# Kernel optimization log

Hardware: AMD Instinct MI355X
Metric: run time of the kernel (lower is better)

Reference implementation:

```python
import jax, jax.numpy as jnp
import numpy as np


def _demosaic_kernels():
    kgrb = 1/8 * np.array([[0,0,-1,0,0],[0,0,2,0,0],[-1,2,4,2,-1],[0,0,2,0,0],[0,0,-1,0,0]], dtype=np.float32)
    krbg0 = 1/8 * np.array([[0,0,0.5,0,0],[0,-1,0,-1,0],[-1,4,5,4,-1],[0,-1,0,-1,0],[0,0,0.5,0,0]], dtype=np.float32)
    krbg1 = krbg0.T
    krbbr = 1/8 * np.array([[0,0,-1.5,0,0],[0,2,0,2,0],[-1.5,0,6,0,-1.5],[0,2,0,2,0],[0,0,-1.5,0,0]], dtype=np.float32)
    return jnp.asarray(np.stack([kgrb, krbg0, krbg1, krbbr], 0)[:, None, :, :])  # (4,1,5,5)


def setup_inputs() -> dict:
    key = jax.random.key(0)
    x = jax.random.uniform(key, (4, 1, 2048, 2048), dtype=jnp.float32)  # RGGB bayer mosaic
    k = _demosaic_kernels()
    return {"x": x, "k": k}


def reference(x, k):
    # reflect-pad by 2 on H and W, then fixed 4-filter 5x5 conv
    xp = jnp.pad(x, ((0, 0), (0, 0), (2, 2), (2, 2)), mode="reflect")
    cfa = jax.lax.conv_general_dilated(
        xp, k, window_strides=(1, 1), padding="VALID",
        dimension_numbers=("NCHW", "OIHW", "NCHW"))  # (N,4,H,W)
    out = jnp.tile(x, (1, 3, 1, 1))  # (N,3,H,W)
    # green at R and B sites
    out = out.at[:, 1, 0::2, 0::2].set(cfa[:, 0, 0::2, 0::2])
    out = out.at[:, 1, 1::2, 1::2].set(cfa[:, 0, 1::2, 1::2])
    # red at G/B sites
    out = out.at[:, 0, 0::2, 1::2].set(cfa[:, 1, 0::2, 1::2])
    out = out.at[:, 0, 1::2, 0::2].set(cfa[:, 2, 1::2, 0::2])
    out = out.at[:, 0, 1::2, 1::2].set(cfa[:, 3, 1::2, 1::2])
    # blue at G/R sites
    out = out.at[:, 2, 0::2, 1::2].set(cfa[:, 2, 0::2, 1::2])
    out = out.at[:, 2, 1::2, 0::2].set(cfa[:, 1, 1::2, 0::2])
    out = out.at[:, 2, 0::2, 0::2].set(cfa[:, 3, 0::2, 0::2])
    return jnp.clip(out, 0.0, 1.0)
```

## Files before the change

### kernel.cpp

```cpp
#include <hip/hip_runtime.h>

#define IMG_H 2048
#define IMG_W 2048
#define NIMG 4

__device__ __forceinline__ int refl(int i, int n) {
    i = (i < 0) ? -i : i;
    return (i >= n) ? (2 * n - 2 - i) : i;
}

__device__ __forceinline__ float clamp01(float v) {
    return fminf(fmaxf(v, 0.0f), 1.0f);
}

__device__ __forceinline__ void px_rgb(
    float x0,
    float xl, float xr, float xll, float xrr,
    float xu, float xd, float xuu, float xdd,
    float dul, float dur, float ddl, float ddr,
    int pr, int pc,
    float& R, float& G, float& B)
{
    float h1 = xl + xr, v1 = xu + xd;
    float h2 = xll + xrr, v2 = xuu + xdd;
    float diag = dul + dur + ddl + ddr;
    float cfa0 = 0.125f * (4.0f * x0 + 2.0f * (h1 + v1) - (h2 + v2));
    float cfa1 = 0.125f * (5.0f * x0 + 4.0f * h1 - h2 + 0.5f * v2 - diag);
    float cfa2 = 0.125f * (5.0f * x0 + 4.0f * v1 - v2 + 0.5f * h2 - diag);
    float cfa3 = 0.125f * (6.0f * x0 + 2.0f * diag - 1.5f * (h2 + v2));

    if (pr == 0) {
        if (pc == 0) { R = x0;   G = cfa0; B = cfa3; }
        else         { R = cfa1; G = x0;   B = cfa2; }
    } else {
        if (pc == 0) { R = cfa2; G = x0;   B = cfa1; }
        else         { R = cfa3; G = cfa0; B = x0;   }
    }
    R = clamp01(R); G = clamp01(G); B = clamp01(B);
}

__global__ __launch_bounds__(256) void demosaic_interior(
    const float* __restrict__ x, float* __restrict__ out)
{
    int idx = blockIdx.x * blockDim.x + threadIdx.x;
    int c4   = idx & 511;
    int rest = idx >> 9;
    int rp   = rest & 1023;
    int n    = rest >> 10;
    if (rp == 0 || rp == 1023 || c4 == 0 || c4 == 511) return;
    int r = rp << 1;
    int c = c4 << 2;

    const float* p = x + (size_t)n * IMG_H * IMG_W;
    const size_t plane = (size_t)IMG_H * IMG_W;
    size_t ob = (size_t)n * 3 * plane + (size_t)r * IMG_W + c;

    const float* b = p + (size_t)r * IMG_W + c;
    float4 m2  = *(const float4*)(b - 2 * IMG_W);
    float4 m1l = *(const float4*)(b - IMG_W - 4);
    float4 m1c = *(const float4*)(b - IMG_W);
    float4 m1r = *(const float4*)(b - IMG_W + 4);
    float4 z0l = *(const float4*)(b - 4);
    float4 z0c = *(const float4*)(b);
    float4 z0r = *(const float4*)(b + 4);
    float4 z1l = *(const float4*)(b + IMG_W - 4);
    float4 z1c = *(const float4*)(b + IMG_W);
    float4 z1r = *(const float4*)(b + IMG_W + 4);
    float4 z2l = *(const float4*)(b + 2 * IMG_W - 4);
    float4 z2c = *(const float4*)(b + 2 * IMG_W);
    float4 z2r = *(const float4*)(b + 2 * IMG_W + 4);
    float4 p3  = *(const float4*)(b + 3 * IMG_W);

    float wm2[4] = {m2.x, m2.y, m2.z, m2.w};
    float wm1[6] = {m1l.w, m1c.x, m1c.y, m1c.z, m1c.w, m1r.x};
    float w0[8]  = {z0l.z, z0l.w, z0c.x, z0c.y, z0c.z, z0c.w, z0r.x, z0r.y};
    float w1[8]  = {z1l.z, z1l.w, z1c.x, z1c.y, z1c.z, z1c.w, z1r.x, z1r.y};
    float w2[6]  = {z2l.w, z2c.x, z2c.y, z2c.z, z2c.w, z2r.x};
    float w3[4]  = {p3.x, p3.y, p3.z, p3.w};

    float R0[4], G0[4], B0[4], R1[4], G1[4], B1[4];
    #pragma unroll
    for (int j = 0; j < 4; j++) {
        px_rgb(w0[j + 2],
               w0[j + 1], w0[j + 3], w0[j], w0[j + 4],
               wm1[j + 1], w1[j + 2], wm2[j], w2[j + 1],
               wm1[j], wm1[j + 2], w1[j + 1], w1[j + 3],
               0, j & 1, R0[j], G0[j], B0[j]);
        px_rgb(w1[j + 2],
               w1[j + 1], w1[j + 3], w1[j], w1[j + 4],
               w0[j + 2], w2[j + 1], wm1[j + 1], w3[j],
               w0[j + 1], w0[j + 3], w2[j], w2[j + 2],
               1, j & 1, R1[j], G1[j], B1[j]);
    }

    *(float4*)(out + ob)                     = make_float4(R0[0], R0[1], R0[2], R0[3]);
    *(float4*)(out + ob + plane)             = make_float4(G0[0], G0[1], G0[2], G0[3]);
    *(float4*)(out + ob + 2 * plane)         = make_float4(B0[0], B0[1], B0[2], B0[3]);
    *(float4*)(out + ob + IMG_W)             = make_float4(R1[0], R1[1], R1[2], R1[3]);
    *(float4*)(out + ob + IMG_W + plane)     = make_float4(G1[0], G1[1], G1[2], G1[3]);
    *(float4*)(out + ob + IMG_W + 2 * plane) = make_float4(B1[0], B1[1], B1[2], B1[3]);
}

__global__ __launch_bounds__(256) void demosaic_border(
    const float* __restrict__ x, float* __restrict__ out)
{
    const int PER_IMG = 1024 + 2044;
    int idx = blockIdx.x * blockDim.x + threadIdx.x;
    if (idx >= NIMG * PER_IMG) return;
    int n = idx / PER_IMG;
    int t = idx - n * PER_IMG;
    int rp, c4;
    if (t < 1024) { rp = (t >> 9) * 1023; c4 = t & 511; }
    else          { int j = t - 1024; rp = 1 + (j >> 1); c4 = (j & 1) * 511; }
    int r = rp << 1;
    int c = c4 << 2;

    const float* p = x + (size_t)n * IMG_H * IMG_W;
    const size_t plane = (size_t)IMG_H * IMG_W;
    size_t ob = (size_t)n * 3 * plane + (size_t)r * IMG_W + c;

    #pragma unroll
    for (int i = 0; i < 2; i++) {
        int rr = r + i;
        int rm1 = refl(rr - 1, IMG_H), rm2 = refl(rr - 2, IMG_H);
        int rp1 = refl(rr + 1, IMG_H), rp2 = refl(rr + 2, IMG_H);
        const float* p0r  = p + (size_t)rr  * IMG_W;
        const float* pm1r = p + (size_t)rm1 * IMG_W;
        const float* pm2r = p + (size_t)rm2 * IMG_W;
        const float* pp1r = p + (size_t)rp1 * IMG_W;
        const float* pp2r = p + (size_t)rp2 * IMG_W;
        #pragma unroll
        for (int j = 0; j < 4; j++) {
            int cc  = c + j;
            int cm1 = refl(cc - 1, IMG_W), cm2 = refl(cc - 2, IMG_W);
            int cp1 = refl(cc + 1, IMG_W), cp2 = refl(cc + 2, IMG_W);
            float R, G, B;
            px_rgb(p0r[cc],
                   p0r[cm1], p0r[cp1], p0r[cm2], p0r[cp2],
                   pm1r[cc], pp1r[cc], pm2r[cc], pp2r[cc],
                   pm1r[cm1], pm1r[cp1], pp1r[cm1], pp1r[cp1],
                   i, cc & 1, R, G, B);
            size_t o = ob + (size_t)i * IMG_W + j;
            out[o]             = R;
            out[o + plane]     = G;
            out[o + 2 * plane] = B;
        }
    }
}

extern "C" void kernel_launch(void* const* d_in, const int* in_sizes, int n_in,
                              void* d_out, int out_size, void* d_ws, size_t ws_size,
                              hipStream_t stream) {
    const float* x = (const float*)d_in[0];
    float* out = (float*)d_out;

    const int total = NIMG * (IMG_H / 2) * (IMG_W / 4);
    demosaic_interior<<<dim3(total / 256), dim3(256), 0, stream>>>(x, out);

    const int btotal = NIMG * (1024 + 2044);
    demosaic_border<<<dim3((btotal + 255) / 256), dim3(256), 0, stream>>>(x, out);
}
```

Before: 262.0 us.

## Merge interior and border kernels into one launch with XCD-aware block remapping

Combines the interior and border demosaic kernels into a single launch that dispatches on block index, removing one kernel launch and the gap between the two. Interior blocks are remapped so consecutive block IDs, which go round-robin to the 8 XCDs, cover contiguous image regions per XCD, so neighbouring rows share each XCD's L2. The border path's loops are no longer unrolled, keeping register pressure low in the shared kernel. Output stores are reordered by plane. The border work is tiny, so most of any effect should come from launch overhead and cache locality.

```diff
diff --git a/kernel.cpp b/kernel.cpp
--- a/kernel.cpp
+++ b/kernel.cpp
@@ -3,6 +3,12 @@
 #define IMG_H 2048
 #define IMG_W 2048
 #define NIMG 4
+#define NXCD 8
+
+#define NBLK_INT (NIMG * (IMG_H / 2) * (IMG_W / 4) / 256)
+#define PER_IMG  (1024 + 2044)
+#define NBORDER  (NIMG * PER_IMG)
+#define NBLK_BOR ((NBORDER + 255) / 256)
 
 __device__ __forceinline__ int refl(int i, int n) {
     i = (i < 0) ? -i : i;
@@ -39,111 +45,118 @@
     R = clamp01(R); G = clamp01(G); B = clamp01(B);
 }
 
-__global__ __launch_bounds__(256) void demosaic_interior(
+__global__ __launch_bounds__(256) void demosaic(
     const float* __restrict__ x, float* __restrict__ out)
 {
-    int idx = blockIdx.x * blockDim.x + threadIdx.x;
-    int c4   = idx & 511;
-    int rest = idx >> 9;
-    int rp   = rest & 1023;
-    int n    = rest >> 10;
-    if (rp == 0 || rp == 1023 || c4 == 0 || c4 == 511) return;
-    int r = rp << 1;
-    int c = c4 << 2;
+    const size_t plane = (size_t)IMG_H * IMG_W;
+    int bid = blockIdx.x;
 
-    const float* p = x + (size_t)n * IMG_H * IMG_W;
-    const size_t plane = (size_t)IMG_H * IMG_W;
-    size_t ob = (size_t)n * 3 * plane + (size_t)r * IMG_W + c;
+    if (bid < NBLK_INT) {
+        int nb  = (bid & (NXCD - 1)) * (NBLK_INT / NXCD) + (bid >> 3);
+        int idx = nb * 256 + (int)threadIdx.x;
 
-    const float* b = p + (size_t)r * IMG_W + c;
-    float4 m2  = *(const float4*)(b - 2 * IMG_W);
-    float4 m1l = *(const float4*)(b - IMG_W - 4);
-    float4 m1c = *(const float4*)(b - IMG_W);
-    float4 m1r = *(const float4*)(b - IMG_W + 4);
-    float4 z0l = *(const float4*)(b - 4);
-    float4 z0c = *(const float4*)(b);
-    float4 z0r = *(const float4*)(b + 4);
-    float4 z1l = *(const float4*)(b + IMG_W - 4);
-    float4 z1c = *(const float4*)(b + IMG_W);
-    float4 z1r = *(const float4*)(b + IMG_W + 4);
-    float4 z2l = *(const float4*)(b + 2 * IMG_W - 4);
-    float4 z2c = *(const float4*)(b + 2 * IMG_W);
-    float4 z2r = *(const float4*)(b + 2 * IMG_W + 4);
-    float4 p3  = *(const float4*)(b + 3 * IMG_W);
+        int c4   = idx & 511;
+        int rest = idx >> 9;
+        int rp   = rest & 1023;
+        int n    = rest >> 10;
+        if (rp == 0 || rp == 1023 || c4 == 0 || c4 == 511) return;
+        int r = rp << 1;
+        int c = c4 << 2;
 
-    float wm2[4] = {m2.x, m2.y, m2.z, m2.w};
-    float wm1[6] = {m1l.w, m1c.x, m1c.y, m1c.z, m1c.w, m1r.x};
-    float w0[8]  = {z0l.z, z0l.w, z0c.x, z0c.y, z0c.z, z0c.w, z0r.x, z0r.y};
-    float w1[8]  = {z1l.z, z1l.w, z1c.x, z1c.y, z1c.z, z1c.w, z1r.x, z1r.y};
-    float w2[6]  = {z2l.w, z2c.x, z2c.y, z2c.z, z2c.w, z2r.x};
-    float w3[4]  = {p3.x, p3.y, p3.z, p3.w};
+        const float* p = x + (size_t)n * IMG_H * IMG_W;
+        size_t ob = (size_t)n * 3 * plane + (size_t)r * IMG_W + c;
 
-    float R0[4], G0[4], B0[4], R1[4], G1[4], B1[4];
-    #pragma unroll
-    for (int j = 0; j < 4; j++) {
-        px_rgb(w0[j + 2],
-               w0[j + 1], w0[j + 3], w0[j], w0[j + 4],
-               wm1[j + 1], w1[j + 2], wm2[j], w2[j + 1],
-               wm1[j], wm1[j + 2], w1[j + 1], w1[j + 3],
-               0, j & 1, R0[j], G0[j], B0[j]);
-        px_rgb(w1[j + 2],
-               w1[j + 1], w1[j + 3], w1[j], w1[j + 4],
-               w0[j + 2], w2[j + 1], wm1[j + 1], w3[j],
-               w0[j + 1], w0[j + 3], w2[j], w2[j + 2],
-               1, j & 1, R1[j], G1[j], B1[j]);
-    }
+        const float* b = p + (size_t)r * IMG_W + c;
+        float4 m2  = *(const float4*)(b - 2 * IMG_W);
+        float4 m1l = *(const float4*)(b - IMG_W - 4);
+        float4 m1c = *(const float4*)(b - IMG_W);
+        float4 m1r = *(const float4*)(b - IMG_W + 4);
+        float4 z0l = *(const float4*)(b - 4);
+        float4 z0c = *(const float4*)(b);
+        float4 z0r = *(const float4*)(b + 4);
+        float4 z1l = *(const float4*)(b + IMG_W - 4);
+        float4 z1c = *(const float4*)(b + IMG_W);
+        float4 z1r = *(const float4*)(b + IMG_W + 4);
+        float4 z2l = *(const float4*)(b + 2 * IMG_W - 4);
+        float4 z2c = *(const float4*)(b + 2 * IMG_W);
+        float4 z2r = *(const float4*)(b + 2 * IMG_W + 4);
+        float4 p3  = *(const float4*)(b + 3 * IMG_W);
 
-    *(float4*)(out + ob)                     = make_float4(R0[0], R0[1], R0[2], R0[3]);
-    *(float4*)(out + ob + plane)             = make_float4(G0[0], G0[1], G0[2], G0[3]);
-    *(float4*)(out + ob + 2 * plane)         = make_float4(B0[0], B0[1], B0[2], B0[3]);
-    *(float4*)(out + ob + IMG_W)             = make_float4(R1[0], R1[1], R1[2], R1[3]);
-    *(float4*)(out + ob + IMG_W + plane)     = make_float4(G1[0], G1[1], G1[2], G1[3]);
-    *(float4*)(out + ob + IMG_W + 2 * plane) = make_float4(B1[0], B1[1], B1[2], B1[3]);
-}
+        float wm2[4] = {m2.x, m2.y, m2.z, m2.w};
+        float wm1[6] = {m1l.w, m1c.x, m1c.y, m1c.z, m1c.w, m1r.x};
+        float w0[8]  = {z0l.z, z0l.w, z0c.x, z0c.y, z0c.z, z0c.w, z0r.x, z0r.y};
+        float w1[8]  = {z1l.z, z1l.w, z1c.x, z1c.y, z1c.z, z1c.w, z1r.x, z1r.y};
+        float w2[6]  = {z2l.w, z2c.x, z2c.y, z2c.z, z2c.w, z2r.x};
+        float w3[4]  = {p3.x, p3.y, p3.z, p3.w};
 
-__global__ __launch_bounds__(256) void demosaic_border(
-    const float* __restrict__ x, float* __restrict__ out)
-{
-    const int PER_IMG = 1024 + 2044;
-    int idx = blockIdx.x * blockDim.x + threadIdx.x;
-    if (idx >= NIMG * PER_IMG) return;
-    int n = idx / PER_IMG;
-    int t = idx - n * PER_IMG;
-    int rp, c4;
-    if (t < 1024) { rp = (t >> 9) * 1023; c4 = t & 511; }
-    else          { int j = t - 1024; rp = 1 + (j >> 1); c4 = (j & 1) * 511; }
-    int r = rp << 1;
-    int c = c4 << 2;
-
-    const float* p = x + (size_t)n * IMG_H * IMG_W;
-    const size_t plane = (size_t)IMG_H * IMG_W;
-    size_t ob = (size_t)n * 3 * plane + (size_t)r * IMG_W + c;
-
-    #pragma unroll
-    for (int i = 0; i < 2; i++) {
-        int rr = r + i;
-        int rm1 = refl(rr - 1, IMG_H), rm2 = refl(rr - 2, IMG_H);
-        int rp1 = refl(rr + 1, IMG_H), rp2 = refl(rr + 2, IMG_H);
-        const float* p0r  = p + (size_t)rr  * IMG_W;
-        const float* pm1r = p + (size_t)rm1 * IMG_W;
-        const float* pm2r = p + (size_t)rm2 * IMG_W;
-        const float* pp1r = p + (size_t)rp1 * IMG_W;
-        const float* pp2r = p + (size_t)rp2 * IMG_W;
+        float R0[4], G0[4], B0[4], R1[4], G1[4], B1[4];
         #pragma unroll
         for (int j = 0; j < 4; j++) {
-            int cc  = c + j;
-            int cm1 = refl(cc - 1, IMG_W), cm2 = refl(cc - 2, IMG_W);
-            int cp1 = refl(cc + 1, IMG_W), cp2 = refl(cc + 2, IMG_W);
-            float R, G, B;
-            px_rgb(p0r[cc],
-                   p0r[cm1], p0r[cp1], p0r[cm2], p0r[cp2],
-                   pm1r[cc], pp1r[cc], pm2r[cc], pp2r[cc],
-                   pm1r[cm1], pm1r[cp1], pp1r[cm1], pp1r[cp1],
-                   i, cc & 1, R, G, B);
-            size_t o = ob + (size_t)i * IMG_W + j;
-            out[o]             = R;
-            out[o + plane]     = G;
-            out[o + 2 * plane] = B;
+            px_rgb(w0[j + 2],
+                   w0[j + 1], w0[j + 3], w0[j], w0[j + 4],
+                   wm1[j + 1], w1[j + 2], wm2[j], w2[j + 1],
+                   wm1[j], wm1[j + 2], w1[j + 1], w1[j + 3],
+                   0, j & 1, R0[j], G0[j], B0[j]);
+            px_rgb(w1[j + 2],
+                   w1[j + 1], w1[j + 3], w1[j], w1[j + 4],
+                   w0[j + 2], w2[j + 1], wm1[j + 1], w3[j],
+                   w0[j + 1], w0[j + 3], w2[j], w2[j + 2],
+                   1, j & 1, R1[j], G1[j], B1[j]);
+        }
+
+        *(float4*)(out + ob)                     = make_float4(R0[0], R0[1], R0[2], R0[3]);
+        *(float4*)(out + ob + IMG_W)             = make_float4(R1[0], R1[1], R1[2], R1[3]);
+        *(float4*)(out + ob + plane)             = make_float4(G0[0], G0[1], G0[2], G0[3]);
+        *(float4*)(out + ob + plane + IMG_W)     = make_float4(G1[0], G1[1], G1[2], G1[3]);
+        *(float4*)(out + ob + 2 * plane)         = make_float4(B0[0], B0[1], B0[2], B0[3]);
+        *(float4*)(out + ob + 2 * plane + IMG_W) = make_float4(B1[0], B1[1], B1[2], B1[3]);
+    } else {
+        int idx = (bid - NBLK_INT) * 256 + (int)threadIdx.x;
+        if (idx >= NBORDER) return;
+        int n = idx / PER_IMG;
+        int t = idx - n * PER_IMG;
+        int rp, c4;
+        if (t < 1024) { rp = (t >> 9) * 1023; c4 = t & 511; }
+        else          { int j = t - 1024; rp = 1 + (j >> 1); c4 = (j & 1) * 511; }
+        int r = rp << 1;
+        int c = c4 << 2;
+
+        const float* p = x + (size_t)n * IMG_H * IMG_W;
+        size_t ob = (size_t)n * 3 * plane + (size_t)r * IMG_W + c;
+
+        #pragma unroll 1
+        for (int i = 0; i < 2; i++) {
+            int rr = r + i;
+            int rm1 = refl(rr - 1, IMG_H), rm2 = refl(rr - 2, IMG_H);
+            int rp1 = refl(rr + 1, IMG_H), rp2 = refl(rr + 2, IMG_H);
+            const float* p0r  = p + (size_t)rr  * IMG_W;
+            const float* pm1r = p + (size_t)rm1 * IMG_W;
+            const float* pm2r = p + (size_t)rm2 * IMG_W;
+            const float* pp1r = p + (size_t)rp1 * IMG_W;
+            const float* pp2r = p + (size_t)rp2 * IMG_W;
+            #pragma unroll 1
+            for (int j = 0; j < 4; j++) {
+                int cc  = c + j;
+                int cm1 = refl(cc - 1, IMG_W), cm2 = refl(cc - 2, IMG_W);
+                int cp1 = refl(cc + 1, IMG_W), cp2 = refl(cc + 2, IMG_W);
+                float R, G, B;
+                if (i == 0)
+                    px_rgb(p0r[cc],
+                           p0r[cm1], p0r[cp1], p0r[cm2], p0r[cp2],
+                           pm1r[cc], pp1r[cc], pm2r[cc], pp2r[cc],
+                           pm1r[cm1], pm1r[cp1], pp1r[cm1], pp1r[cp1],
+                           0, cc & 1, R, G, B);
+                else
+                    px_rgb(p0r[cc],
+                           p0r[cm1], p0r[cp1], p0r[cm2], p0r[cp2],
+                           pm1r[cc], pp1r[cc], pm2r[cc], pp2r[cc],
+                           pm1r[cm1], pm1r[cp1], pp1r[cm1], pp1r[cp1],
+                           1, cc & 1, R, G, B);
+                size_t o = ob + (size_t)i * IMG_W + j;
+                out[o]             = R;
+                out[o + plane]     = G;
+                out[o + 2 * plane] = B;
+            }
         }
     }
 }
@@ -154,9 +167,5 @@
     const float* x = (const float*)d_in[0];
     float* out = (float*)d_out;
 
-    const int total = NIMG * (IMG_H / 2) * (IMG_W / 4);
-    demosaic_interior<<<dim3(total / 256), dim3(256), 0, stream>>>(x, out);
-
-    const int btotal = NIMG * (1024 + 2044);
-    demosaic_border<<<dim3((btotal + 255) / 256), dim3(256), 0, stream>>>(x, out);
+    demosaic<<<dim3(NBLK_INT + NBLK_BOR), dim3(256), 0, stream>>>(x, out);
 }
```

Result: slower. 275.6 us (+5.2%).
